# Kernel optimization log

Measured on AMD Instinct MI355X. Metric: run time of the kernel, lower is better.

Reference implementation:

```python
import math
import jax, jax.numpy as jnp
import numpy as np

B, L, E, H = 8, 1024, 512, 8
HD = E // H  # head_dim = 64
P = 2 * L - 1  # relative position length


def setup_inputs() -> dict:
    key = jax.random.key(0)
    ks = jax.random.split(key, 9)
    s = 0.02  # xavier-ish scale for params
    return {
        "x": jax.random.normal(ks[0], (B, L, E), jnp.float32),
        "pos_embs": jax.random.normal(ks[1], (1, P, E), jnp.float32),
        "in_proj_weight": jax.random.normal(ks[2], (3 * E, E), jnp.float32) * s,
        "linear_pos_w": jax.random.normal(ks[3], (E, E), jnp.float32) * s,
        "out_proj_w": jax.random.normal(ks[4], (E, E), jnp.float32) * s,
        "out_proj_b": jnp.zeros((E,), jnp.float32),
        "pos_bias_u": jax.random.normal(ks[5], (HD, H), jnp.float32) * s,
        "pos_bias_v": jax.random.normal(ks[6], (HD, H), jnp.float32) * s,
    }


def rel_shift(t):
    # Transformer-XL relative shift: pad/reshape/slice trick.
    b, h, q, p = t.shape  # p = 2*klen - 1
    t = jnp.pad(t, ((0, 0), (0, 0), (0, 0), (1, 0)))
    t = t.reshape(b, h, p + 1, q)[:, :, 1:, :].reshape(b, h, q, p)
    return t[..., : p // 2 + 1]  # (b, h, q, klen)


def reference(x, pos_embs, in_proj_weight, linear_pos_w, out_proj_w, out_proj_b,
              pos_bias_u, pos_bias_v):
    bsz, qlen, _ = x.shape
    scale = 1.0 / math.sqrt(E)  # note: 1/sqrt(embed_dim), not head_dim

    # fused qkv projection; torch chunks along the last dim of (B,L,H,3*HD)
    proj = (x @ in_proj_weight.T).reshape(bsz, qlen, H, 3 * HD)
    q, k, v = jnp.split(proj, 3, axis=-1)  # each (B,L,H,HD)

    # positional keys
    p_k = (pos_embs @ linear_pos_w.T).reshape(-1, H, HD)  # (P,H,HD)

    # pos_bias_u is stored (HD,H) and .view(H,HD)'d in torch -> plain reshape
    u = pos_bias_u.reshape(H, HD)
    vb = pos_bias_v.reshape(H, HD)

    matrix_ac = jnp.einsum('bqhd,bkhd->bhqk', (q + u) * scale, k)
    matrix_bd = jnp.einsum('bqhd,phd->bhqp', (q + vb) * scale, p_k)
    matrix_bd = rel_shift(matrix_bd)  # (B,H,L,L)

    attn = jax.nn.softmax((matrix_ac + matrix_bd).astype(jnp.float32), axis=-1)

    ctx = jnp.einsum('bhqk,bkhd->bqhd', attn, v).reshape(bsz, qlen, E)
    out = ctx @ out_proj_w.T + out_proj_b
    return out, attn
```

## Files before the change

kernel.cpp:

```cpp
#include <hip/hip_runtime.h>
#include <math.h>

#define BB 8
#define LL 1024
#define EE 512
#define HH 8
#define HD 64
#define PP 2047

static constexpr float SCALE = 0.04419417382415922f;

typedef __bf16 bf16x8 __attribute__((ext_vector_type(8)));
typedef float f32x4 __attribute__((ext_vector_type(4)));
typedef unsigned short u16;
typedef u16 u16x8 __attribute__((ext_vector_type(8)));

#define MFMA16(a, b, c) __builtin_amdgcn_mfma_f32_16x16x32_bf16(a, b, c, 0, 0, 0)

static __device__ __forceinline__ unsigned short f2bfbits(float f) {
    union { float f; unsigned u; } v; v.f = f;
    unsigned r = v.u + 0x7fffu + ((v.u >> 16) & 1u);
    return (unsigned short)(r >> 16);
}
static __device__ __forceinline__ float bfbits2f(unsigned short b) {
    union { unsigned u; float f; } v; v.u = ((unsigned)b) << 16;
    return v.f;
}

static __device__ __forceinline__ u16x8 cvt8(float4 lo, float4 hi) {
    u16x8 r;
    r[0] = f2bfbits(lo.x); r[1] = f2bfbits(lo.y);
    r[2] = f2bfbits(lo.z); r[3] = f2bfbits(lo.w);
    r[4] = f2bfbits(hi.x); r[5] = f2bfbits(hi.y);
    r[6] = f2bfbits(hi.z); r[7] = f2bfbits(hi.w);
    return r;
}

template<bool CLAMP>
static __device__ __forceinline__ void gemm128(
    const float* __restrict__ Ag, const float* __restrict__ Bg,
    int m0, int n0, int amax, u16* As, u16* Bs, f32x4 (&acc)[4][4])
{
    const int tid = threadIdx.x;
    const int w = tid >> 6, lane = tid & 63;
    const int g = lane >> 4, c16 = lane & 15;
    const int wr = w >> 1, wc = w & 1;
    const int srow = tid >> 3, su = tid & 7;

#pragma unroll
    for (int i = 0; i < 4; i++)
#pragma unroll
        for (int j = 0; j < 4; j++) acc[i][j] = (f32x4){0.f, 0.f, 0.f, 0.f};

    for (int kt = 0; kt < EE; kt += 64) {
        float4 al[4], ah[4], bl[4], bh[4];
#pragma unroll
        for (int ps = 0; ps < 4; ps++) {
            int row = ps * 32 + srow;
            int ar = m0 + row;
            if (CLAMP) ar = ar > amax ? amax : ar;
            const float* ap = Ag + (size_t)ar * EE + kt + su * 8;
            al[ps] = *(const float4*)ap;
            ah[ps] = *(const float4*)(ap + 4);
            const float* bp = Bg + (size_t)(n0 + row) * EE + kt + su * 8;
            bl[ps] = *(const float4*)bp;
            bh[ps] = *(const float4*)(bp + 4);
        }
        __syncthreads();
#pragma unroll
        for (int ps = 0; ps < 4; ps++) {
            int row = ps * 32 + srow;
            int off = row * 64 + ((su ^ (row & 7)) << 3);
            *(u16x8*)&As[off] = cvt8(al[ps], ah[ps]);
            *(u16x8*)&Bs[off] = cvt8(bl[ps], bh[ps]);
        }
        __syncthreads();
#pragma unroll
        for (int kk = 0; kk < 2; kk++) {
            bf16x8 av[4], bv[4];
#pragma unroll
            for (int mt = 0; mt < 4; mt++) {
                int r0 = wr * 64 + mt * 16 + c16;
                av[mt] = *(const bf16x8*)&As[r0 * 64 + (((kk * 4 + g) ^ (r0 & 7)) << 3)];
            }
#pragma unroll
            for (int nt = 0; nt < 4; nt++) {
                int r0 = wc * 64 + nt * 16 + c16;
                bv[nt] = *(const bf16x8*)&Bs[r0 * 64 + (((kk * 4 + g) ^ (r0 & 7)) << 3)];
            }
#pragma unroll
            for (int mt = 0; mt < 4; mt++)
#pragma unroll
                for (int nt = 0; nt < 4; nt++)
                    acc[mt][nt] = MFMA16(av[mt], bv[nt], acc[mt][nt]);
        }
    }
}

__global__ __launch_bounds__(256) void qkv_kernel(
    const float* __restrict__ x,
    const float* __restrict__ wq,
    const float* __restrict__ ubias,
    const float* __restrict__ vbias,
    unsigned short* __restrict__ Qu,
    unsigned short* __restrict__ Qv,
    unsigned short* __restrict__ Kw,
    unsigned short* __restrict__ Vt)
{
    __shared__ u16 As[128 * 64];
    __shared__ u16 Bs[128 * 64];
    const int m0 = blockIdx.y * 128, n0 = blockIdx.x * 128;
    f32x4 acc[4][4];
    gemm128<false>(x, wq, m0, n0, 0, As, Bs, acc);

    const int tid = threadIdx.x;
    const int w = tid >> 6, lane = tid & 63;
    const int g = lane >> 4, c16 = lane & 15;
    const int wr = w >> 1, wc = w & 1;

#pragma unroll
    for (int mt = 0; mt < 4; mt++) {
#pragma unroll
        for (int r = 0; r < 4; r++) {
            int m = m0 + wr * 64 + mt * 16 + g * 4 + r;
            int b = m >> 10, l = m & 1023;
#pragma unroll
            for (int nt = 0; nt < 4; nt++) {
                int n = n0 + wc * 64 + nt * 16 + c16;
                int h = n / 192;
                int rr = n - h * 192;
                int cls = rr >> 6;
                int d = rr & 63;
                float v = acc[mt][nt][r];
                if (cls == 0) {
                    size_t idx = ((size_t)(b * HH + h) * LL + l) * HD + d;
                    Qu[idx] = f2bfbits((v + ubias[h * 64 + d]) * SCALE);
                    Qv[idx] = f2bfbits((v + vbias[h * 64 + d]) * SCALE);
                } else if (cls == 1) {
                    Kw[((size_t)(b * HH + h) * LL + l) * HD + d] = f2bfbits(v);
                } else {
                    Vt[((size_t)(b * HH + h) * HD + d) * LL + l] = f2bfbits(v);
                }
            }
        }
    }
}

__global__ __launch_bounds__(256) void posk_kernel(
    const float* __restrict__ pe,
    const float* __restrict__ wp,
    unsigned short* __restrict__ pko)
{
    __shared__ u16 As[128 * 64];
    __shared__ u16 Bs[128 * 64];
    const int m0 = blockIdx.y * 128, n0 = blockIdx.x * 128;
    f32x4 acc[4][4];
    gemm128<true>(pe, wp, m0, n0, PP - 1, As, Bs, acc);

    const int tid = threadIdx.x;
    const int w = tid >> 6, lane = tid & 63;
    const int g = lane >> 4, c16 = lane & 15;
    const int wr = w >> 1, wc = w & 1;

#pragma unroll
    for (int mt = 0; mt < 4; mt++) {
#pragma unroll
        for (int r = 0; r < 4; r++) {
            int p = m0 + wr * 64 + mt * 16 + g * 4 + r;
            if (p >= PP) continue;
#pragma unroll
            for (int nt = 0; nt < 4; nt++) {
                int n = n0 + wc * 64 + nt * 16 + c16;
                int h = n >> 6, d = n & 63;
                pko[((size_t)h * PP + p) * HD + d] = f2bfbits(acc[mt][nt][r]);
            }
        }
    }
}

__global__ __launch_bounds__(256) void outproj_kernel(
    const float* __restrict__ ctx,
    const float* __restrict__ wo,
    const float* __restrict__ bias,
    float* __restrict__ out)
{
    __shared__ u16 As[128 * 64];
    __shared__ u16 Bs[128 * 64];
    const int m0 = blockIdx.y * 128, n0 = blockIdx.x * 128;
    f32x4 acc[4][4];
    gemm128<false>(ctx, wo, m0, n0, 0, As, Bs, acc);

    const int tid = threadIdx.x;
    const int w = tid >> 6, lane = tid & 63;
    const int g = lane >> 4, c16 = lane & 15;
    const int wr = w >> 1, wc = w & 1;

#pragma unroll
    for (int mt = 0; mt < 4; mt++) {
#pragma unroll
        for (int r = 0; r < 4; r++) {
            int m = m0 + wr * 64 + mt * 16 + g * 4 + r;
#pragma unroll
            for (int nt = 0; nt < 4; nt++) {
                int n = n0 + wc * 64 + nt * 16 + c16;
                out[(size_t)m * EE + n] = acc[mt][nt][r] + bias[n];
            }
        }
    }
}

__global__ __launch_bounds__(256, 3) void attn_kernel(
    const unsigned short* __restrict__ Qu, const unsigned short* __restrict__ Qv,
    const unsigned short* __restrict__ Kw, const unsigned short* __restrict__ Vt,
    const unsigned short* __restrict__ pk,
    float* __restrict__ attn,
    float* __restrict__ ctx)
{
    const int b = blockIdx.z, h = blockIdx.y, q0 = blockIdx.x * 16;
    const int tid = threadIdx.x;
    const int w = tid >> 6, lane = tid & 63;
    const int g = lane >> 4, c16 = lane & 15;
    const int bh = b * HH + h;

    __shared__ unsigned short BDG[4][16 * 152];
    __shared__ float SMmax[4][16];
    __shared__ float SMsum[4][16];
    __shared__ float CTX[4][16 * 68];

    const unsigned short* qub = Qu + ((size_t)bh * LL + q0 + c16) * HD + g * 8;
    const unsigned short* qvb = Qv + ((size_t)bh * LL + q0 + c16) * HD + g * 8;
    bf16x8 au0 = *(const bf16x8*)qub;
    bf16x8 au1 = *(const bf16x8*)(qub + 32);
    bf16x8 av0 = *(const bf16x8*)qvb;
    bf16x8 av1 = *(const bf16x8*)(qvb + 32);

    f32x4 lg[16];
#pragma unroll
    for (int t = 0; t < 16; t++) lg[t] = (f32x4){0.f, 0.f, 0.f, 0.f};

    const unsigned short* kbase  = Kw + (size_t)bh * LL * HD;
    const unsigned short* pkbase = pk + (size_t)h * PP * HD;

#pragma unroll
    for (int p = 0; p < 2; p++) {
        const int kp = w * 256 + p * 128;
        const int pstart = kp - q0 + 1008;
#pragma unroll
        for (int ct = 0; ct < 9; ct++) {
            int prow = pstart + ct * 16 + c16;
            prow = prow > (PP - 1) ? (PP - 1) : prow;
            const unsigned short* pb = pkbase + (size_t)prow * HD + g * 8;
            f32x4 acc = (f32x4){0.f, 0.f, 0.f, 0.f};
            acc = MFMA16(av0, *(const bf16x8*)pb, acc);
            acc = MFMA16(av1, *(const bf16x8*)(pb + 32), acc);
#pragma unroll
            for (int r = 0; r < 4; r++)
                BDG[w][(g * 4 + r) * 152 + ct * 16 + c16] = f2bfbits(acc[r]);
        }
#pragma unroll
        for (int jt = 0; jt < 8; jt++) {
            const unsigned short* kb = kbase + (size_t)(kp + jt * 16 + c16) * HD + g * 8;
            int t = p * 8 + jt;
            lg[t] = MFMA16(au0, *(const bf16x8*)kb, lg[t]);
            lg[t] = MFMA16(au1, *(const bf16x8*)(kb + 32), lg[t]);
        }
        __syncthreads();
#pragma unroll
        for (int jt = 0; jt < 8; jt++) {
            int t = p * 8 + jt;
#pragma unroll
            for (int r = 0; r < 4; r++) {
                int i = g * 4 + r;
                int c = jt * 16 + c16 - i + 15;
                lg[t][r] += bfbits2f(BDG[w][i * 152 + c]);
            }
        }
        __syncthreads();
    }

    float M[4], Sv[4], inv[4];
#pragma unroll
    for (int r = 0; r < 4; r++) {
        float m = lg[0][r];
#pragma unroll
        for (int t = 1; t < 16; t++) m = fmaxf(m, lg[t][r]);
        M[r] = m;
    }
#pragma unroll
    for (int off = 8; off >= 1; off >>= 1)
#pragma unroll
        for (int r = 0; r < 4; r++) M[r] = fmaxf(M[r], __shfl_xor(M[r], off, 16));
    if (c16 == 0) {
#pragma unroll
        for (int r = 0; r < 4; r++) SMmax[w][g * 4 + r] = M[r];
    }
    __syncthreads();
#pragma unroll
    for (int r = 0; r < 4; r++) {
        int row = g * 4 + r;
        M[r] = fmaxf(fmaxf(SMmax[0][row], SMmax[1][row]),
                     fmaxf(SMmax[2][row], SMmax[3][row]));
        Sv[r] = 0.f;
    }
#pragma unroll
    for (int t = 0; t < 16; t++)
#pragma unroll
        for (int r = 0; r < 4; r++) {
            float e = __expf(lg[t][r] - M[r]);
            lg[t][r] = e;
            Sv[r] += e;
        }
#pragma unroll
    for (int off = 8; off >= 1; off >>= 1)
#pragma unroll
        for (int r = 0; r < 4; r++) Sv[r] += __shfl_xor(Sv[r], off, 16);
    if (c16 == 0) {
#pragma unroll
        for (int r = 0; r < 4; r++) SMsum[w][g * 4 + r] = Sv[r];
    }
    __syncthreads();
#pragma unroll
    for (int r = 0; r < 4; r++) {
        int row = g * 4 + r;
        inv[r] = 1.0f / (SMsum[0][row] + SMsum[1][row] + SMsum[2][row] + SMsum[3][row]);
    }

    float* arow = attn + (size_t)bh * LL * LL;
#pragma unroll
    for (int t = 0; t < 16; t++)
#pragma unroll
        for (int r = 0; r < 4; r++) {
            float pr = lg[t][r] * inv[r];
            lg[t][r] = pr;
            arow[(size_t)(q0 + g * 4 + r) * LL + w * 256 + t * 16 + c16] = pr;
        }

    f32x4 cacc[4];
#pragma unroll
    for (int nt = 0; nt < 4; nt++) cacc[nt] = (f32x4){0.f, 0.f, 0.f, 0.f};

#pragma unroll
    for (int p = 0; p < 2; p++) {
        const int kp = w * 256 + p * 128;
        __syncthreads();
#pragma unroll
        for (int jt = 0; jt < 8; jt++) {
            int t = p * 8 + jt;
#pragma unroll
            for (int r = 0; r < 4; r++)
                BDG[w][(g * 4 + r) * 152 + jt * 16 + c16] = f2bfbits(lg[t][r]);
        }
        __syncthreads();
        bf16x8 pa[4];
#pragma unroll
        for (int kk = 0; kk < 4; kk++)
            pa[kk] = *(const bf16x8*)&BDG[w][c16 * 152 + kk * 32 + g * 8];
#pragma unroll
        for (int kk = 0; kk < 4; kk++) {
#pragma unroll
            for (int nt = 0; nt < 4; nt++) {
                const unsigned short* vb =
                    Vt + ((size_t)bh * HD + nt * 16 + c16) * LL + kp + kk * 32 + g * 8;
                cacc[nt] = MFMA16(pa[kk], *(const bf16x8*)vb, cacc[nt]);
            }
        }
    }

    __syncthreads();
#pragma unroll
    for (int nt = 0; nt < 4; nt++)
#pragma unroll
        for (int r = 0; r < 4; r++)
            CTX[w][(g * 4 + r) * 68 + nt * 16 + c16] = cacc[nt][r];
    __syncthreads();
    {
        int row = tid >> 4, d4 = (tid & 15) * 4;
        f32x4 s = *(const f32x4*)&CTX[0][row * 68 + d4];
        s += *(const f32x4*)&CTX[1][row * 68 + d4];
        s += *(const f32x4*)&CTX[2][row * 68 + d4];
        s += *(const f32x4*)&CTX[3][row * 68 + d4];
        *(f32x4*)&ctx[((size_t)b * LL + q0 + row) * EE + h * HD + d4] = s;
    }
}

extern "C" void kernel_launch(void* const* d_in, const int* in_sizes, int n_in,
                              void* d_out, int out_size, void* d_ws, size_t ws_size,
                              hipStream_t stream)
{
    const float* x   = (const float*)d_in[0];
    const float* pe  = (const float*)d_in[1];
    const float* ipw = (const float*)d_in[2];
    const float* lpw = (const float*)d_in[3];
    const float* opw = (const float*)d_in[4];
    const float* opb = (const float*)d_in[5];
    const float* pbu = (const float*)d_in[6];
    const float* pbv = (const float*)d_in[7];

    float* out  = (float*)d_out;
    float* attn = (float*)d_out + (size_t)BB * LL * EE;

    const size_t NQ = (size_t)BB * HH * LL * HD;
    float* ctx = (float*)d_ws;
    unsigned short* wsu = (unsigned short*)(ctx + (size_t)BB * LL * EE);
    unsigned short* Qu = wsu; wsu += NQ;
    unsigned short* Qv = wsu; wsu += NQ;
    unsigned short* Kw = wsu; wsu += NQ;
    unsigned short* Vt = wsu; wsu += NQ;
    unsigned short* pkb = wsu; wsu += (size_t)HH * PP * HD;

    qkv_kernel<<<dim3(12, 64), 256, 0, stream>>>(x, ipw, pbu, pbv, Qu, Qv, Kw, Vt);
    posk_kernel<<<dim3(4, 16), 256, 0, stream>>>(pe, lpw, pkb);
    attn_kernel<<<dim3(64, 8, 8), 256, 0, stream>>>(Qu, Qv, Kw, Vt, pkb, attn, ctx);
    outproj_kernel<<<dim3(4, 64), 256, 0, stream>>>(ctx, opw, opb, out);
}
```

Baseline: 566.6 us.

## Pre-cast GEMM operands to bf16 and load tiles via global_load_lds

Adds a cast kernel that converts x, pos_embs and the three weight matrices to bf16 once per call, and makes the attention kernel write ctx in bf16. The projection GEMMs then stream bf16 tiles straight into LDS with global_load_lds, replacing the fp32 load, convert and ds_write staging path. This halves operand bytes read by the GEMMs and removes per-tile conversion work, at the cost of an extra launch and a full read and write pass over the inputs. It also adds a trailing barrier per k-step and still uses a single LDS buffer, so loads do not overlap compute.

```diff
diff --git a/kernel.cpp b/kernel.cpp
--- a/kernel.cpp
+++ b/kernel.cpp
@@ -14,6 +14,7 @@
 typedef float f32x4 __attribute__((ext_vector_type(4)));
 typedef unsigned short u16;
 typedef u16 u16x8 __attribute__((ext_vector_type(8)));
+typedef u16 u16x4 __attribute__((ext_vector_type(4)));
 
 #define MFMA16(a, b, c) __builtin_amdgcn_mfma_f32_16x16x32_bf16(a, b, c, 0, 0, 0)
 
@@ -36,43 +37,65 @@
     return r;
 }
 
+static __device__ __forceinline__ void gload_lds16(const u16* g, u16* l) {
+    __builtin_amdgcn_global_load_lds(
+        (const __attribute__((address_space(1))) unsigned int*)g,
+        (__attribute__((address_space(3))) unsigned int*)l, 16, 0, 0);
+}
+
+__global__ __launch_bounds__(256) void cast_all(
+    const float* __restrict__ x, const float* __restrict__ pe,
+    const float* __restrict__ ipw, const float* __restrict__ lpw,
+    const float* __restrict__ opw,
+    u16* __restrict__ Xb, u16* __restrict__ Pb, u16* __restrict__ Wqb,
+    u16* __restrict__ Wpb, u16* __restrict__ Wob)
+{
+    size_t e = ((size_t)blockIdx.x * 256 + threadIdx.x) * 8;
+    const float* src; u16* dst; size_t off;
+    if (e < 4194304)      { src = x;   dst = Xb;  off = e; }
+    else if (e < 5242368) { src = pe;  dst = Pb;  off = e - 4194304; }
+    else if (e < 6028800) { src = ipw; dst = Wqb; off = e - 5242368; }
+    else if (e < 6290944) { src = lpw; dst = Wpb; off = e - 6028800; }
+    else if (e < 6553088) { src = opw; dst = Wob; off = e - 6290944; }
+    else return;
+    float4 lo = *(const float4*)&src[off];
+    float4 hi = *(const float4*)&src[off + 4];
+    *(u16x8*)&dst[off] = cvt8(lo, hi);
+}
+
 template<bool CLAMP>
-static __device__ __forceinline__ void gemm128(
-    const float* __restrict__ Ag, const float* __restrict__ Bg,
+static __device__ __forceinline__ void gemm128b(
+    const u16* __restrict__ Ab, const u16* __restrict__ Bb,
     int m0, int n0, int amax, u16* As, u16* Bs, f32x4 (&acc)[4][4])
 {
     const int tid = threadIdx.x;
     const int w = tid >> 6, lane = tid & 63;
     const int g = lane >> 4, c16 = lane & 15;
     const int wr = w >> 1, wc = w & 1;
-    const int srow = tid >> 3, su = tid & 7;
 
 #pragma unroll
     for (int i = 0; i < 4; i++)
 #pragma unroll
         for (int j = 0; j < 4; j++) acc[i][j] = (f32x4){0.f, 0.f, 0.f, 0.f};
 
+    int arow[4], brow[4], cs8[4], ldsu[4];
+#pragma unroll
+    for (int j = 0; j < 4; j++) {
+        int U = j * 256 + tid;
+        int row = U >> 3, cu = U & 7;
+        cs8[j] = (cu ^ (row & 7)) * 8;
+        int ar = m0 + row;
+        if (CLAMP) ar = ar > amax ? amax : ar;
+        arow[j] = ar;
+        brow[j] = n0 + row;
+        ldsu[j] = (j * 256 + (w << 6)) * 8;
+    }
+
     for (int kt = 0; kt < EE; kt += 64) {
-        float4 al[4], ah[4], bl[4], bh[4];
-#pragma unroll
-        for (int ps = 0; ps < 4; ps++) {
-            int row = ps * 32 + srow;
-            int ar = m0 + row;
-            if (CLAMP) ar = ar > amax ? amax : ar;
-            const float* ap = Ag + (size_t)ar * EE + kt + su * 8;
-            al[ps] = *(const float4*)ap;
-            ah[ps] = *(const float4*)(ap + 4);
-            const float* bp = Bg + (size_t)(n0 + row) * EE + kt + su * 8;
-            bl[ps] = *(const float4*)bp;
-            bh[ps] = *(const float4*)(bp + 4);
-        }
-        __syncthreads();
-#pragma unroll
-        for (int ps = 0; ps < 4; ps++) {
-            int row = ps * 32 + srow;
-            int off = row * 64 + ((su ^ (row & 7)) << 3);
-            *(u16x8*)&As[off] = cvt8(al[ps], ah[ps]);
-            *(u16x8*)&Bs[off] = cvt8(bl[ps], bh[ps]);
+#pragma unroll
+        for (int j = 0; j < 4; j++) {
+            gload_lds16(Ab + (size_t)arow[j] * EE + kt + cs8[j], As + ldsu[j]);
+            gload_lds16(Bb + (size_t)brow[j] * EE + kt + cs8[j], Bs + ldsu[j]);
         }
         __syncthreads();
 #pragma unroll
@@ -94,12 +117,13 @@
                 for (int nt = 0; nt < 4; nt++)
                     acc[mt][nt] = MFMA16(av[mt], bv[nt], acc[mt][nt]);
         }
+        __syncthreads();
     }
 }
 
 __global__ __launch_bounds__(256) void qkv_kernel(
-    const float* __restrict__ x,
-    const float* __restrict__ wq,
+    const u16* __restrict__ xb,
+    const u16* __restrict__ wq,
     const float* __restrict__ ubias,
     const float* __restrict__ vbias,
     unsigned short* __restrict__ Qu,
@@ -111,7 +135,7 @@
     __shared__ u16 Bs[128 * 64];
     const int m0 = blockIdx.y * 128, n0 = blockIdx.x * 128;
     f32x4 acc[4][4];
-    gemm128<false>(x, wq, m0, n0, 0, As, Bs, acc);
+    gemm128b<false>(xb, wq, m0, n0, 0, As, Bs, acc);
 
     const int tid = threadIdx.x;
     const int w = tid >> 6, lane = tid & 63;
@@ -147,15 +171,15 @@
 }
 
 __global__ __launch_bounds__(256) void posk_kernel(
-    const float* __restrict__ pe,
-    const float* __restrict__ wp,
+    const u16* __restrict__ peb,
+    const u16* __restrict__ wp,
     unsigned short* __restrict__ pko)
 {
     __shared__ u16 As[128 * 64];
     __shared__ u16 Bs[128 * 64];
     const int m0 = blockIdx.y * 128, n0 = blockIdx.x * 128;
     f32x4 acc[4][4];
-    gemm128<true>(pe, wp, m0, n0, PP - 1, As, Bs, acc);
+    gemm128b<true>(peb, wp, m0, n0, PP - 1, As, Bs, acc);
 
     const int tid = threadIdx.x;
     const int w = tid >> 6, lane = tid & 63;
@@ -179,8 +203,8 @@
 }
 
 __global__ __launch_bounds__(256) void outproj_kernel(
-    const float* __restrict__ ctx,
-    const float* __restrict__ wo,
+    const u16* __restrict__ ctxb,
+    const u16* __restrict__ wo,
     const float* __restrict__ bias,
     float* __restrict__ out)
 {
@@ -188,7 +212,7 @@
     __shared__ u16 Bs[128 * 64];
     const int m0 = blockIdx.y * 128, n0 = blockIdx.x * 128;
     f32x4 acc[4][4];
-    gemm128<false>(ctx, wo, m0, n0, 0, As, Bs, acc);
+    gemm128b<false>(ctxb, wo, m0, n0, 0, As, Bs, acc);
 
     const int tid = threadIdx.x;
     const int w = tid >> 6, lane = tid & 63;
@@ -214,7 +238,7 @@
     const unsigned short* __restrict__ Kw, const unsigned short* __restrict__ Vt,
     const unsigned short* __restrict__ pk,
     float* __restrict__ attn,
-    float* __restrict__ ctx)
+    u16* __restrict__ ctxb)
 {
     const int b = blockIdx.z, h = blockIdx.y, q0 = blockIdx.x * 16;
     const int tid = threadIdx.x;
@@ -379,7 +403,10 @@
         s += *(const f32x4*)&CTX[1][row * 68 + d4];
         s += *(const f32x4*)&CTX[2][row * 68 + d4];
         s += *(const f32x4*)&CTX[3][row * 68 + d4];
-        *(f32x4*)&ctx[((size_t)b * LL + q0 + row) * EE + h * HD + d4] = s;
+        u16x4 o;
+        o[0] = f2bfbits(s[0]); o[1] = f2bfbits(s[1]);
+        o[2] = f2bfbits(s[2]); o[3] = f2bfbits(s[3]);
+        *(u16x4*)&ctxb[((size_t)b * LL + q0 + row) * EE + h * HD + d4] = o;
     }
 }
 
@@ -400,16 +427,22 @@
     float* attn = (float*)d_out + (size_t)BB * LL * EE;
 
     const size_t NQ = (size_t)BB * HH * LL * HD;
-    float* ctx = (float*)d_ws;
-    unsigned short* wsu = (unsigned short*)(ctx + (size_t)BB * LL * EE);
-    unsigned short* Qu = wsu; wsu += NQ;
-    unsigned short* Qv = wsu; wsu += NQ;
-    unsigned short* Kw = wsu; wsu += NQ;
-    unsigned short* Vt = wsu; wsu += NQ;
-    unsigned short* pkb = wsu; wsu += (size_t)HH * PP * HD;
-
-    qkv_kernel<<<dim3(12, 64), 256, 0, stream>>>(x, ipw, pbu, pbv, Qu, Qv, Kw, Vt);
-    posk_kernel<<<dim3(4, 16), 256, 0, stream>>>(pe, lpw, pkb);
-    attn_kernel<<<dim3(64, 8, 8), 256, 0, stream>>>(Qu, Qv, Kw, Vt, pkb, attn, ctx);
-    outproj_kernel<<<dim3(4, 64), 256, 0, stream>>>(ctx, opw, opb, out);
-}
+    u16* wsu  = (u16*)d_ws;
+    u16* ctxb = wsu; wsu += (size_t)BB * LL * EE;
+    u16* Qu   = wsu; wsu += NQ;
+    u16* Qv   = wsu; wsu += NQ;
+    u16* Kw   = wsu; wsu += NQ;
+    u16* Vt   = wsu; wsu += NQ;
+    u16* pkb  = wsu; wsu += (size_t)HH * PP * HD;
+    u16* Xb   = wsu; wsu += 4194304;
+    u16* Pb   = wsu; wsu += 1048064;
+    u16* Wqb  = wsu; wsu += 786432;
+    u16* Wpb  = wsu; wsu += 262144;
+    u16* Wob  = wsu; wsu += 262144;
+
+    cast_all<<<3200, 256, 0, stream>>>(x, pe, ipw, lpw, opw, Xb, Pb, Wqb, Wpb, Wob);
+    qkv_kernel<<<dim3(12, 64), 256, 0, stream>>>(Xb, Wqb, pbu, pbv, Qu, Qv, Kw, Vt);
+    posk_kernel<<<dim3(4, 16), 256, 0, stream>>>(Pb, Wpb, pkb);
+    attn_kernel<<<dim3(64, 8, 8), 256, 0, stream>>>(Qu, Qv, Kw, Vt, pkb, attn, ctxb);
+    outproj_kernel<<<dim3(4, 64), 256, 0, stream>>>(ctxb, opw ? Wob : Wob, opb, out);
+}
```

After: 541.2 us. 1.05x faster.
